# Kernel tuning notes

Hardware: AMD Instinct MI355X
Metric: run time of the kernel (lower is better)

## Reference

```python
import jax, jax.numpy as jnp
from jax import lax
import numpy as np

B = 16384
EPS = 1e-5


def conv2d(x, w, b, pad):
    # x: [N,C,H,W], w: [O,I,kh,kw]
    y = lax.conv_general_dilated(x, w, (1, 1), [(pad, pad), (pad, pad)],
                                 dimension_numbers=("NCHW", "OIHW", "NCHW"))
    return y + b[None, :, None, None]


def maxpool2(x):
    return lax.reduce_window(x, -jnp.inf, lax.max, (1, 1, 2, 2), (1, 1, 2, 2), "VALID")


def setup_inputs() -> dict:
    key = jax.random.key(0)
    ks = jax.random.split(key, 16)
    n = jax.random.normal
    return {
        "x": n(ks[0], (B, 1, 28, 28), dtype=jnp.float32),
        "conv1_w": n(ks[1], (8, 1, 3, 3), dtype=jnp.float32) * 0.2,
        "conv1_b": n(ks[2], (8,), dtype=jnp.float32) * 0.1,
        "conv2_w": n(ks[3], (16, 8, 3, 3), dtype=jnp.float32) * 0.1,
        "conv2_b": n(ks[4], (16,), dtype=jnp.float32) * 0.1,
        "s1_w": n(ks[5], (4, 2), dtype=jnp.float32) * 0.5,
        "s1_b": n(ks[6], (4,), dtype=jnp.float32) * 0.1,
        "s2_w": n(ks[7], (2, 4), dtype=jnp.float32) * 0.5,
        "s2_b": n(ks[8], (2,), dtype=jnp.float32) * 0.1,
        "filt_w": n(ks[9], (1, 1, 2, 2), dtype=jnp.float32) * 0.5,
        "filt_b": n(ks[10], (1,), dtype=jnp.float32) * 0.1,
        "fc1_w": n(ks[11], (64, 787), dtype=jnp.float32) * 0.03,
        "fc1_b": n(ks[12], (64,), dtype=jnp.float32) * 0.1,
        "fc2_w": n(ks[13], (4, 64), dtype=jnp.float32) * 0.1,
        "fc2_b": n(ks[14], (4,), dtype=jnp.float32) * 0.1,
        "bn_g": jnp.ones((4,), dtype=jnp.float32),
        "bn_b": jnp.zeros((4,), dtype=jnp.float32),
    }


def reference(x, conv1_w, conv1_b, conv2_w, conv2_b, s1_w, s1_b, s2_w, s2_b,
              filt_w, filt_b, fc1_w, fc1_b, fc2_w, fc2_b, bn_g, bn_b):
    bsz = x.shape[0]
    # feature extractor: conv3x3 -> relu -> maxpool2 (x2)
    f = maxpool2(jax.nn.relu(conv2d(x, conv1_w, conv1_b, 1)))        # [B,8,14,14]
    f = maxpool2(jax.nn.relu(conv2d(f, conv2_w, conv2_b, 1)))        # [B,16,7,7]
    flat = f.reshape(bsz, -1)                                        # [B,784]
    # sampler on first two features
    h = jnp.tanh(flat[:, :2] @ s1_w.T + s1_b)
    sampler_out = jax.nn.softmax(h @ s2_w.T + s2_b, axis=-1)         # [B,2]
    # conv filter: 2x2 stride-1 conv + sigmoid, mean over all patches
    logits = conv2d(x, filt_w, filt_b, 0)                            # [B,1,27,27]
    conv_out = jnp.mean(jax.nn.sigmoid(logits), axis=(1, 2, 3))[:, None]  # [B,1]
    combined = jnp.concatenate([flat, sampler_out, conv_out], axis=1)  # [B,787]
    out = jax.nn.relu(combined @ fc1_w.T + fc1_b) @ fc2_w.T + fc2_b    # [B,4]
    # BatchNorm1d, training mode (batch stats, biased variance)
    mu = jnp.mean(out, axis=0)
    var = jnp.var(out, axis=0)
    return (out - mu) * lax.rsqrt(var + EPS) * bn_g + bn_b
```

## Files before the change

kernel.cpp:

```cpp
#include <hip/hip_runtime.h>
#include <hip/hip_fp16.h>
#include <math.h>

#define NBATCH 16384
#define EPSV 1e-5f
#define IMGW 4

typedef short short8 __attribute__((ext_vector_type(8)));
typedef _Float16 half8_t __attribute__((ext_vector_type(8)));
typedef short short2v __attribute__((ext_vector_type(2)));
typedef float f32x4 __attribute__((ext_vector_type(4)));
union V8 { uint4 u; short8 s; };
union VH { uint4 u; half8_t h; };

__device__ __forceinline__ unsigned short f2bf(float f) {
    unsigned int x = __float_as_uint(f);
    return (unsigned short)((x + 0x7fffu + ((x >> 16) & 1u)) >> 16);
}
__device__ __forceinline__ __half2 u2h(unsigned int u) { return __builtin_bit_cast(__half2, u); }
__device__ __forceinline__ unsigned int h2u(__half2 h) { return __builtin_bit_cast(unsigned int, h); }

__global__ __launch_bounds__(256) void k_prep(
    const float* __restrict__ fc1w, const float* __restrict__ w2,
    const float* __restrict__ w1, const float* __restrict__ b1,
    unsigned short* __restrict__ wt, unsigned short* __restrict__ af16,
    unsigned int* __restrict__ w1h2, unsigned int* __restrict__ b1h2)
{
    int i = blockIdx.x * 256 + threadIdx.x;
    if (i < 51200) {
        int n = i / 800, k = i - n * 800;
        float v = (k < 787) ? fc1w[n * 787 + k] : 0.f;
        wt[i] = f2bf(v);
    } else if (i < 52736) {
        int a = i - 51200;
        int slot = a >> 7, rem = a & 127, oc = rem >> 3, ic = rem & 7;
        float v = (slot < 9) ? w2[oc * 72 + ic * 9 + slot] : 0.f;
        af16[a] = __half_as_ushort(__float2half(v));
    } else if (i < 52808) {
        int k = i - 52736;
        unsigned int hb = __half_as_ushort(__float2half(w1[k]));
        w1h2[k] = hb | (hb << 16);
    } else if (i < 52816) {
        int k = i - 52808;
        unsigned int hb = __half_as_ushort(__float2half(b1[k]));
        b1h2[k] = hb | (hb << 16);
    }
}

__global__ __launch_bounds__(256) void k_conv(
    const float* __restrict__ x,
    const float* __restrict__ s1w, const float* __restrict__ s1b,
    const float* __restrict__ s2w, const float* __restrict__ s2b,
    const float* __restrict__ fw, const float* __restrict__ fb,
    const float* __restrict__ b2,
    const unsigned short* __restrict__ Afg,
    const unsigned int* __restrict__ w1h2g,
    const unsigned int* __restrict__ b1h2g,
    unsigned short* __restrict__ comb)
{
    const int t = threadIdx.x;
    const int w = t >> 6, l = t & 63;

    __shared__ unsigned int sxu_all[4][30 * 18];
    __shared__ __align__(16) unsigned short sf1_all[4][16 * 136];
    __shared__ __align__(16) float scomb_all[4][800];
    __shared__ float ssm[27];
    __shared__ float sb2s[16];

    unsigned int* sxu = sxu_all[w];
    unsigned short* sf1 = sf1_all[w];
    float* scomb = scomb_all[w];

    if (t < 8) ssm[t] = s1w[t];
    else if (t < 12) ssm[t] = s1b[t - 8];
    else if (t < 20) ssm[t] = s2w[t - 12];
    else if (t < 22) ssm[t] = s2b[t - 20];
    else if (t < 26) ssm[t] = fw[t - 22];
    else if (t == 26) ssm[26] = fb[0];
    if (t >= 32 && t < 48) sb2s[t - 32] = b2[t - 32];
    __syncthreads();

    for (int i = l; i < 540; i += 64) sxu[i] = 0u;
    if (l < 60) {
        int R, C;
        if (l < 16)      { R = 0;      C = l; }
        else if (l < 32) { R = 15;     C = l - 16; }
        else if (l < 46) { R = l - 31; C = 0; }
        else             { R = l - 45; C = 15; }
        *reinterpret_cast<uint4*>(&sf1[R * 136 + C * 8]) = uint4{0u, 0u, 0u, 0u};
    }
    if (l < 16) scomb[784 + l] = 0.f;

    const __half2 fwh0 = __float2half2_rn(ssm[22]);
    const __half2 fwh1 = __float2half2_rn(ssm[23]);
    const __half2 fwh2 = __float2half2_rn(ssm[24]);
    const __half2 fwh3 = __float2half2_rn(ssm[25]);
    const __half2 fbh  = __float2half2_rn(ssm[26]);

    const int n = l & 15, g = l >> 4;
    const int qr = n & 7;
    const int q = (qr < 7) ? qr : 6;
    const int dr = n >> 3;
    int offs[3];
    VH af[3];
    #pragma unroll
    for (int s = 0; s < 3; ++s) {
        const int slot = s * 4 + g;
        const int u = slot / 3, v = slot - 3 * (slot / 3);
        offs[s] = (slot <= 8) ? (u * 136 + v * 8) : 0;
        af[s].u = *reinterpret_cast<const uint4*>(Afg + ((slot * 16 + n) << 3));
    }

    #pragma unroll 1
    for (int img = 0; img < IMGW; ++img) {
        const int b = (blockIdx.x * 4 + w) * IMGW + img;
        const float* xb = x + (size_t)b * 784;

        for (int u0 = l; u0 < 420; u0 += 64) {
            int r = u0 / 15, ww = u0 - (u0 / 15) * 15;
            __half2 h2;
            if (ww == 0)       h2 = __floats2half2_rn(0.f, xb[r * 28]);
            else if (ww == 14) h2 = __floats2half2_rn(xb[r * 28 + 27], 0.f);
            else               h2 = __floats2half2_rn(xb[r * 28 + 2 * ww - 1],
                                                      xb[r * 28 + 2 * ww]);
            sxu[(r + 1) * 18 + ww] = h2u(h2);
        }

        float fsum = 0.f;
        for (int u0 = l; u0 < 378; u0 += 64) {
            int r = u0 / 14, cp = u0 - (u0 / 14) * 14;
            unsigned int A1 = sxu[(r + 1) * 18 + cp], B1 = sxu[(r + 1) * 18 + cp + 1];
            unsigned int A2 = sxu[(r + 2) * 18 + cp], B2 = sxu[(r + 2) * 18 + cp + 1];
            __half2 al1 = u2h(__builtin_amdgcn_alignbit(B1, A1, 16));
            __half2 al2 = u2h(__builtin_amdgcn_alignbit(B2, A2, 16));
            __half2 acc = __hfma2(fwh0, al1,
                          __hfma2(fwh1, u2h(B1),
                          __hfma2(fwh2, al2,
                          __hfma2(fwh3, u2h(B2), fbh))));
            float2 f = __half22float2(acc);
            fsum += __frcp_rn(1.f + __expf(-f.x));
            if (cp < 13) fsum += __frcp_rn(1.f + __expf(-f.y));
        }
        #pragma unroll
        for (int off = 32; off > 0; off >>= 1)
            fsum += __shfl_xor(fsum, off, 64);

        for (int i = l; i < 196; i += 64) {
            const int p = i / 14, j = i - (i / 14) * 14;
            unsigned int A[4], B[4], M[4];
            #pragma unroll
            for (int u = 0; u < 4; ++u) {
                A[u] = sxu[(2 * p + u) * 18 + j];
                B[u] = sxu[(2 * p + u) * 18 + j + 1];
                M[u] = __builtin_amdgcn_alignbit(B[u], A[u], 16);
            }
            unsigned short outv[8];
            #pragma unroll
            for (int oc = 0; oc < 8; ++oc) {
                __half2 a0 = u2h(b1h2g[oc]), a1 = a0;
                #pragma unroll
                for (int u = 0; u < 3; ++u) {
                    #pragma unroll
                    for (int v = 0; v < 3; ++v) {
                        const __half2 wv = u2h(w1h2g[oc * 9 + u * 3 + v]);
                        const unsigned int p0 = (v == 0) ? A[u]     : ((v == 1) ? M[u]     : B[u]);
                        const unsigned int p1 = (v == 0) ? A[u + 1] : ((v == 1) ? M[u + 1] : B[u + 1]);
                        a0 = __hfma2(wv, u2h(p0), a0);
                        a1 = __hfma2(wv, u2h(p1), a1);
                    }
                }
                short2v s0 = __builtin_bit_cast(short2v, a0);
                short2v s1 = __builtin_bit_cast(short2v, a1);
                short2v mm = __builtin_elementwise_max(s0, s1);
                short m = mm[0] > mm[1] ? mm[0] : mm[1];
                if (m < 0) m = 0;
                outv[oc] = (unsigned short)m;
            }
            *reinterpret_cast<uint4*>(&sf1[(p + 1) * 136 + (j + 1) * 8]) =
                *reinterpret_cast<const uint4*>(outv);
        }

        for (int pp = 0; pp < 7; ++pp) {
            const int rbase = (2 * pp + dr) * 136 + (2 * q) * 8;
            f32x4 acc0 = {0.f, 0.f, 0.f, 0.f}, acc1 = {0.f, 0.f, 0.f, 0.f};
            #pragma unroll
            for (int s = 0; s < 3; ++s) {
                VH b0, b1v;
                b0.u  = *reinterpret_cast<const uint4*>(&sf1[rbase + offs[s]]);
                b1v.u = *reinterpret_cast<const uint4*>(&sf1[rbase + 8 + offs[s]]);
                acc0 = __builtin_amdgcn_mfma_f32_16x16x32_f16(af[s].h, b0.h, acc0, 0, 0, 0);
                acc1 = __builtin_amdgcn_mfma_f32_16x16x32_f16(af[s].h, b1v.h, acc1, 0, 0, 0);
            }
            #pragma unroll
            for (int i = 0; i < 4; ++i) {
                const float bias = sb2s[4 * g + i];
                float m = fmaxf(acc0[i], acc1[i]);
                m = fmaxf(m, __shfl_xor(m, 8, 64));
                if (n < 7)
                    scomb[(4 * g + i) * 49 + pp * 7 + q] = fmaxf(m + bias, 0.f);
            }
        }

        if (l == 0) {
            scomb[786] = fsum * (1.f / 729.f);
            float f0 = scomb[0], f1 = scomb[1];
            float h[4];
            #pragma unroll
            for (int k = 0; k < 4; ++k) {
                float y = fmaf(f0, ssm[k * 2], fmaf(f1, ssm[k * 2 + 1], ssm[8 + k]));
                float e = __expf(2.f * y);
                h[k] = (e - 1.f) * __frcp_rn(e + 1.f);
            }
            float l0 = ssm[20], l1 = ssm[21];
            #pragma unroll
            for (int k = 0; k < 4; ++k) {
                l0 = fmaf(h[k], ssm[12 + k], l0);
                l1 = fmaf(h[k], ssm[16 + k], l1);
            }
            float mx = fmaxf(l0, l1);
            float e0 = __expf(l0 - mx), e1 = __expf(l1 - mx);
            float inv = __frcp_rn(e0 + e1);
            scomb[784] = e0 * inv;
            scomb[785] = e1 * inv;
        }

        for (int u = l; u < 100; u += 64) {
            const float4* sp = reinterpret_cast<const float4*>(scomb);
            float4 f0 = sp[2 * u], f1 = sp[2 * u + 1];
            uint4 o;
            o.x = (unsigned int)f2bf(f0.x) | ((unsigned int)f2bf(f0.y) << 16);
            o.y = (unsigned int)f2bf(f0.z) | ((unsigned int)f2bf(f0.w) << 16);
            o.z = (unsigned int)f2bf(f1.x) | ((unsigned int)f2bf(f1.y) << 16);
            o.w = (unsigned int)f2bf(f1.z) | ((unsigned int)f2bf(f1.w) << 16);
            reinterpret_cast<uint4*>(comb)[(size_t)b * 100 + u] = o;
        }
    }
}

__global__ __launch_bounds__(256) void k_fc(
    const unsigned short* __restrict__ A,
    const unsigned short* __restrict__ Bw,
    const float* __restrict__ fc1b,
    const float* __restrict__ fc2w, const float* __restrict__ fc2b,
    float* __restrict__ out, float* __restrict__ part)
{
    __shared__ uint4 Asm[2][256];
    __shared__ uint4 Bsm[2][256];
    __shared__ float sh[64][68];
    __shared__ float sfc2[4][64];
    __shared__ float pacc[4][8];

    const int t = threadIdx.x;
    const int w = t >> 6, l = t & 63;
    const int blk = blockIdx.x;

    sfc2[t >> 6][t & 63] = fc2w[t];

    const int srow = t >> 2, skbp = t & 3;
    const int skbl = skbp ^ ((srow >> 1) & 3);
    const uint4* Ag = reinterpret_cast<const uint4*>(A) + ((size_t)blk * 64 + srow) * 100;
    const uint4* Bg = reinterpret_cast<const uint4*>(Bw) + (size_t)srow * 100;
    const int sidx = srow * 4 + skbp;

    const int arow = w * 16 + (l & 15);
    const int aidx = arow * 4 + ((l >> 4) ^ ((arow >> 1) & 3));
    int bidx[4];
    #pragma unroll
    for (int nf = 0; nf < 4; ++nf) {
        int nn = nf * 16 + (l & 15);
        bidx[nf] = nn * 4 + ((l >> 4) ^ ((nn >> 1) & 3));
    }

    f32x4 acc0 = {0.f, 0.f, 0.f, 0.f}, acc1 = acc0, acc2 = acc0, acc3 = acc0;

    Asm[0][sidx] = Ag[skbl];
    Bsm[0][sidx] = Bg[skbl];

    int buf = 0;
    for (int s = 0; s < 25; ++s) {
        __syncthreads();
        if (s < 24) {
            Asm[buf ^ 1][sidx] = Ag[(s + 1) * 4 + skbl];
            Bsm[buf ^ 1][sidx] = Bg[(s + 1) * 4 + skbl];
        }
        V8 av; av.u = Asm[buf][aidx];
        V8 b0; b0.u = Bsm[buf][bidx[0]];
        V8 b1; b1.u = Bsm[buf][bidx[1]];
        V8 b2; b2.u = Bsm[buf][bidx[2]];
        V8 b3; b3.u = Bsm[buf][bidx[3]];
        acc0 = __builtin_amdgcn_mfma_f32_16x16x32_bf16(av.s, b0.s, acc0, 0, 0, 0);
        acc1 = __builtin_amdgcn_mfma_f32_16x16x32_bf16(av.s, b1.s, acc1, 0, 0, 0);
        acc2 = __builtin_amdgcn_mfma_f32_16x16x32_bf16(av.s, b2.s, acc2, 0, 0, 0);
        acc3 = __builtin_amdgcn_mfma_f32_16x16x32_bf16(av.s, b3.s, acc3, 0, 0, 0);
        buf ^= 1;
    }

    {
        const int c0 = l & 15, r0 = w * 16 + (l >> 4) * 4;
        float fb0 = fc1b[c0], fb1 = fc1b[16 + c0], fb2 = fc1b[32 + c0], fb3 = fc1b[48 + c0];
        #pragma unroll
        for (int r = 0; r < 4; ++r) {
            sh[r0 + r][c0]      = fmaxf(acc0[r] + fb0, 0.f);
            sh[r0 + r][16 + c0] = fmaxf(acc1[r] + fb1, 0.f);
            sh[r0 + r][32 + c0] = fmaxf(acc2[r] + fb2, 0.f);
            sh[r0 + r][48 + c0] = fmaxf(acc3[r] + fb3, 0.f);
        }
    }
    __syncthreads();

    {
        const int row = t >> 2, oo = t & 3;
        float s = fc2b[oo];
        #pragma unroll 8
        for (int o = 0; o < 64; ++o)
            s = fmaf(sh[row][o], sfc2[oo][o], s);
        out[((size_t)blk * 64 + row) * 4 + oo] = s;

        float rs = s, rq = s * s;
        #pragma unroll
        for (int off = 4; off < 64; off <<= 1) {
            rs += __shfl_xor(rs, off, 64);
            rq += __shfl_xor(rq, off, 64);
        }
        if (l < 4) pacc[w][l] = rs;
        else if (l < 8) pacc[w][l] = rq;
    }
    __syncthreads();
    if (t < 8)
        part[blk * 8 + t] = pacc[0][t] + pacc[1][t] + pacc[2][t] + pacc[3][t];
}

__global__ void k_bnfinal(const float* __restrict__ part,
                          const float* __restrict__ g, const float* __restrict__ bb,
                          float* __restrict__ ss, int nblocks)
{
    const int t = threadIdx.x;
    float s[8];
    #pragma unroll
    for (int i = 0; i < 8; ++i) s[i] = 0.f;
    for (int idx = t; idx < nblocks; idx += 64)
        #pragma unroll
        for (int i = 0; i < 8; ++i) s[i] += part[idx * 8 + i];
    #pragma unroll
    for (int i = 0; i < 8; ++i)
        #pragma unroll
        for (int off = 32; off > 0; off >>= 1)
            s[i] += __shfl_xor(s[i], off, 64);
    if (t == 0) {
        const float invB = 1.f / 16384.f;
        #pragma unroll
        for (int j = 0; j < 4; ++j) {
            float mu = s[j] * invB;
            float var = s[4 + j] * invB - mu * mu;
            float sc = g[j] * rsqrtf(var + EPSV);
            ss[j] = sc;
            ss[4 + j] = bb[j] - mu * sc;
        }
    }
}

__global__ __launch_bounds__(256) void k_bnapply(const float* __restrict__ ss,
                                                 float* __restrict__ out)
{
    const int row = blockIdx.x * 256 + threadIdx.x;
    float4 v = reinterpret_cast<float4*>(out)[row];
    v.x = fmaf(v.x, ss[0], ss[4]);
    v.y = fmaf(v.y, ss[1], ss[5]);
    v.z = fmaf(v.z, ss[2], ss[6]);
    v.w = fmaf(v.w, ss[3], ss[7]);
    reinterpret_cast<float4*>(out)[row] = v;
}

__global__ __launch_bounds__(256) void k_transpose_fb(const float* __restrict__ in,
                                                      float* __restrict__ out)
{
    int i = blockIdx.x * 256 + threadIdx.x;
    if (i < 787 * 64) {
        int k = i >> 6, o = i & 63;
        out[i] = in[o * 787 + k];
    }
}

#define SF1F(ic, r, c) sf1[(ic) * 324 + (r) * 20 + (c)]

__global__ __launch_bounds__(256) void k_fused_fb(
    const float* __restrict__ x,
    const float* __restrict__ w1, const float* __restrict__ b1,
    const float* __restrict__ w2, const float* __restrict__ b2,
    const float* __restrict__ s1w, const float* __restrict__ s1b,
    const float* __restrict__ s2w, const float* __restrict__ s2b,
    const float* __restrict__ fw, const float* __restrict__ fb,
    const float* __restrict__ wt, const float* __restrict__ fc1b,
    const float* __restrict__ fc2w, const float* __restrict__ fc2b,
    float* __restrict__ pre)
{
    const int b = blockIdx.x;
    const int t = threadIdx.x;

    __shared__ float sxA[30][20];
    __shared__ float sxB[30][20];
    __shared__ float sf1[8 * 324];
    __shared__ float scomb[788];
    __shared__ float sw1[72];
    __shared__ float sb1[8];
    __shared__ float sw2p[16 * 76];
    __shared__ float sb2[16];
    __shared__ float sh1p[4][64];
    __shared__ float sh1[64];
    __shared__ float sred[4];
    __shared__ float ssm[27];

    for (int i = t; i < 600; i += 256) { (&sxA[0][0])[i] = 0.f; (&sxB[0][0])[i] = 0.f; }
    for (int i = t; i < 8 * 324; i += 256) sf1[i] = 0.f;
    if (t < 72) sw1[t] = w1[t];
    if (t < 8) sb1[t] = b1[t];
    for (int i = t; i < 1152; i += 256) {
        int oc = i / 72, rem = i - oc * 72;
        sw2p[oc * 76 + rem] = w2[i];
    }
    if (t < 16) sb2[t] = b2[t];
    if (t < 8) ssm[t] = s1w[t];
    else if (t < 12) ssm[t] = s1b[t - 8];
    else if (t < 20) ssm[t] = s2w[t - 12];
    else if (t < 22) ssm[t] = s2b[t - 20];
    else if (t < 26) ssm[t] = fw[t - 22];
    else if (t == 26) ssm[t] = fb[0];
    __syncthreads();

    const float* xb = x + (size_t)b * 784;
    for (int i = t; i < 784; i += 256) {
        int r = i / 28, c = i - (i / 28) * 28;
        float v = xb[i];
        int pr = r + 1, pc = c + 1;
        if (pc <= 15) sxA[pr][pc] = v;
        if (pc >= 14) sxB[pr][pc - 14] = v;
    }
    __syncthreads();

    {
        const float fw00 = ssm[22], fw01 = ssm[23], fw10 = ssm[24], fw11 = ssm[25];
        const float fbv = ssm[26];
        float fsum = 0.f;
        for (int i = t; i < 729; i += 256) {
            int r = i / 27, c = i - (i / 27) * 27;
            float x00, x01, x10, x11;
            if (c <= 13) {
                x00 = sxA[r + 1][c + 1]; x01 = sxA[r + 1][c + 2];
                x10 = sxA[r + 2][c + 1]; x11 = sxA[r + 2][c + 2];
            } else {
                int cb = c - 14;
                x00 = sxB[r + 1][cb + 1]; x01 = sxB[r + 1][cb + 2];
                x10 = sxB[r + 2][cb + 1]; x11 = sxB[r + 2][cb + 2];
            }
            float v = fbv;
            v = fmaf(x00, fw00, v); v = fmaf(x01, fw01, v);
            v = fmaf(x10, fw10, v); v = fmaf(x11, fw11, v);
            fsum += 1.f / (1.f + expf(-v));
        }
        #pragma unroll
        for (int off = 32; off > 0; off >>= 1)
            fsum += __shfl_xor(fsum, off, 64);
        if ((t & 63) == 0) sred[t >> 6] = fsum;
    }

    {
        const int half = t >> 7;
        const int id = t & 127;
        if (id < 112) {
            const int p = id >> 3, oc = id & 7;
            const float* base = half ? &sxB[0][0] : &sxA[0][0];
            float X[4][16];
            #pragma unroll
            for (int u = 0; u < 4; ++u) {
                const float4* rp = reinterpret_cast<const float4*>(base + (2 * p + u) * 20);
                float4 a = rp[0], bb4 = rp[1], c4 = rp[2], d4 = rp[3];
                X[u][0] = a.x;  X[u][1] = a.y;  X[u][2] = a.z;  X[u][3] = a.w;
                X[u][4] = bb4.x; X[u][5] = bb4.y; X[u][6] = bb4.z; X[u][7] = bb4.w;
                X[u][8] = c4.x;  X[u][9] = c4.y;  X[u][10] = c4.z; X[u][11] = c4.w;
                X[u][12] = d4.x; X[u][13] = d4.y; X[u][14] = d4.z; X[u][15] = d4.w;
            }
            float W[9];
            #pragma unroll
            for (int k = 0; k < 9; ++k) W[k] = sw1[oc * 9 + k];
            const float bias = sb1[oc];
            const int j0 = half * 7;
            #pragma unroll
            for (int jj = 0; jj < 7; ++jj) {
                float m = 0.f;
                #pragma unroll
                for (int dr = 0; dr < 2; ++dr)
                    #pragma unroll
                    for (int dc = 0; dc < 2; ++dc) {
                        float acc = bias;
                        #pragma unroll
                        for (int u = 0; u < 3; ++u)
                            #pragma unroll
                            for (int v = 0; v < 3; ++v)
                                acc = fmaf(X[dr + u][2 * jj + dc + v], W[u * 3 + v], acc);
                        m = fmaxf(m, acc);
                    }
                SF1F(oc, p + 1, j0 + jj + 1) = m;
            }
        }
    }
    __syncthreads();

    if (t < 112) {
        const int p = t >> 4, oc = t & 15;
        const float bias = sb2[oc];
        float acc[7][4];
        #pragma unroll
        for (int jj = 0; jj < 7; ++jj)
            #pragma unroll
            for (int s = 0; s < 4; ++s) acc[jj][s] = bias;
        for (int ic = 0; ic < 8; ++ic) {
            float X[4][16];
            #pragma unroll
            for (int u = 0; u < 4; ++u) {
                const float4* rp = reinterpret_cast<const float4*>(&SF1F(ic, 2 * p + u, 0));
                float4 a = rp[0], bb4 = rp[1], c4 = rp[2], d4 = rp[3];
                X[u][0] = a.x;  X[u][1] = a.y;  X[u][2] = a.z;  X[u][3] = a.w;
                X[u][4] = bb4.x; X[u][5] = bb4.y; X[u][6] = bb4.z; X[u][7] = bb4.w;
                X[u][8] = c4.x;  X[u][9] = c4.y;  X[u][10] = c4.z; X[u][11] = c4.w;
                X[u][12] = d4.x; X[u][13] = d4.y; X[u][14] = d4.z; X[u][15] = d4.w;
            }
            float W[9];
            #pragma unroll
            for (int k = 0; k < 9; ++k) W[k] = sw2p[oc * 76 + ic * 9 + k];
            #pragma unroll
            for (int jj = 0; jj < 7; ++jj)
                #pragma unroll
                for (int dr = 0; dr < 2; ++dr)
                    #pragma unroll
                    for (int dc = 0; dc < 2; ++dc)
                        #pragma unroll
                        for (int u = 0; u < 3; ++u)
                            #pragma unroll
                            for (int v = 0; v < 3; ++v)
                                acc[jj][dr * 2 + dc] =
                                    fmaf(X[dr + u][2 * jj + dc + v], W[u * 3 + v], acc[jj][dr * 2 + dc]);
        }
        #pragma unroll
        for (int jj = 0; jj < 7; ++jj) {
            float m = fmaxf(fmaxf(acc[jj][0], acc[jj][1]), fmaxf(acc[jj][2], acc[jj][3]));
            scomb[oc * 49 + p * 7 + jj] = fmaxf(m, 0.f);
        }
    }
    __syncthreads();

    if (t == 0) {
        scomb[786] = (sred[0] + sred[1] + sred[2] + sred[3]) * (1.f / 729.f);
        float f0 = scomb[0], f1 = scomb[1];
        float h[4];
        #pragma unroll
        for (int k = 0; k < 4; ++k)
            h[k] = tanhf(fmaf(f0, ssm[k * 2], fmaf(f1, ssm[k * 2 + 1], ssm[8 + k])));
        float l0 = ssm[20], l1 = ssm[21];
        #pragma unroll
        for (int k = 0; k < 4; ++k) {
            l0 = fmaf(h[k], ssm[12 + k], l0);
            l1 = fmaf(h[k], ssm[16 + k], l1);
        }
        float mx = fmaxf(l0, l1);
        float e0 = expf(l0 - mx), e1 = expf(l1 - mx);
        float inv = 1.f / (e0 + e1);
        scomb[784] = e0 * inv;
        scomb[785] = e1 * inv;
    }
    __syncthreads();

    {
        const int o = t & 63, w = t >> 6;
        const int k0 = w * 197;
        const int k1 = (w == 3) ? 787 : k0 + 197;
        const float* wp = wt + (size_t)k0 * 64 + o;
        float acc = 0.f;
        #pragma unroll 4
        for (int k = k0; k < k1; ++k) {
            acc = fmaf(scomb[k], *wp, acc);
            wp += 64;
        }
        sh1p[w][o] = acc;
    }
    __syncthreads();
    if (t < 64)
        sh1[t] = fmaxf(sh1p[0][t] + sh1p[1][t] + sh1p[2][t] + sh1p[3][t] + fc1b[t], 0.f);
    __syncthreads();

    {
        const int oo = t >> 6, lane = t & 63;
        float v = sh1[lane] * fc2w[oo * 64 + lane];
        #pragma unroll
        for (int off = 32; off > 0; off >>= 1)
            v += __shfl_xor(v, off, 64);
        if (lane == 0) pre[(size_t)b * 4 + oo] = v + fc2b[oo];
    }
}

__global__ __launch_bounds__(256) void k_bnstat_fb(const float* __restrict__ pre,
                                                   float* __restrict__ part)
{
    const int t = threadIdx.x;
    const int row = blockIdx.x * 256 + t;
    float4 v = reinterpret_cast<const float4*>(pre)[row];
    float s0 = v.x, s1 = v.y, s2 = v.z, s3 = v.w;
    float q0 = v.x * v.x, q1 = v.y * v.y, q2 = v.z * v.z, q3 = v.w * v.w;
    #pragma unroll
    for (int off = 32; off > 0; off >>= 1) {
        s0 += __shfl_xor(s0, off, 64);
        s1 += __shfl_xor(s1, off, 64);
        s2 += __shfl_xor(s2, off, 64);
        s3 += __shfl_xor(s3, off, 64);
        q0 += __shfl_xor(q0, off, 64);
        q1 += __shfl_xor(q1, off, 64);
        q2 += __shfl_xor(q2, off, 64);
        q3 += __shfl_xor(q3, off, 64);
    }
    __shared__ float acc[4][8];
    if ((t & 63) == 0) {
        int w = t >> 6;
        acc[w][0] = s0; acc[w][1] = s1; acc[w][2] = s2; acc[w][3] = s3;
        acc[w][4] = q0; acc[w][5] = q1; acc[w][6] = q2; acc[w][7] = q3;
    }
    __syncthreads();
    if (t < 8)
        part[blockIdx.x * 8 + t] = acc[0][t] + acc[1][t] + acc[2][t] + acc[3][t];
}

extern "C" void kernel_launch(void* const* d_in, const int* in_sizes, int n_in,
                              void* d_out, int out_size, void* d_ws, size_t ws_size,
                              hipStream_t stream)
{
    const float* x    = (const float*)d_in[0];
    const float* w1   = (const float*)d_in[1];
    const float* b1   = (const float*)d_in[2];
    const float* w2   = (const float*)d_in[3];
    const float* b2   = (const float*)d_in[4];
    const float* s1w  = (const float*)d_in[5];
    const float* s1b  = (const float*)d_in[6];
    const float* s2w  = (const float*)d_in[7];
    const float* s2b  = (const float*)d_in[8];
    const float* fw   = (const float*)d_in[9];
    const float* fb   = (const float*)d_in[10];
    const float* fc1w = (const float*)d_in[11];
    const float* fc1b = (const float*)d_in[12];
    const float* fc2w = (const float*)d_in[13];
    const float* fc2b = (const float*)d_in[14];
    const float* bng  = (const float*)d_in[15];
    const float* bnb  = (const float*)d_in[16];

    float* out = (float*)d_out;

    const size_t COMB_BYTES = (size_t)NBATCH * 800 * 2;
    const size_t WT_BYTES   = 64 * 800 * 2;
    const size_t AF16_BYTES = 1536 * 2;
    const size_t W1H2_BYTES = 72 * 4;
    const size_t B1H2_BYTES = 8 * 4;
    const size_t PART_BYTES = 256 * 8 * 4;
    const size_t NEED = COMB_BYTES + WT_BYTES + AF16_BYTES + W1H2_BYTES +
                        B1H2_BYTES + PART_BYTES + 32;

    if (ws_size >= NEED) {
        char* p = (char*)d_ws;
        unsigned short* comb = (unsigned short*)p;                     p += COMB_BYTES;
        unsigned short* wtbf = (unsigned short*)p;                     p += WT_BYTES;
        unsigned short* af16 = (unsigned short*)p;                     p += AF16_BYTES;
        unsigned int*   w1h2 = (unsigned int*)p;                       p += W1H2_BYTES;
        unsigned int*   b1h2 = (unsigned int*)p;                       p += B1H2_BYTES;
        float*          part = (float*)p;                              p += PART_BYTES;
        float*          ss   = (float*)p;

        k_prep<<<207, 256, 0, stream>>>(fc1w, w2, w1, b1, wtbf, af16, w1h2, b1h2);
        k_conv<<<NBATCH / (4 * IMGW), 256, 0, stream>>>(x, s1w, s1b, s2w, s2b, fw, fb, b2,
                                                        af16, w1h2, b1h2, comb);
        k_fc<<<256, 256, 0, stream>>>(comb, wtbf, fc1b, fc2w, fc2b, out, part);
        k_bnfinal<<<1, 64, 0, stream>>>(part, bng, bnb, ss, 256);
        k_bnapply<<<64, 256, 0, stream>>>(ss, out);
    } else {
        float* part = (float*)d_ws;
        float* ss   = part + 512;
        float* wt   = ss + 8;

        k_transpose_fb<<<197, 256, 0, stream>>>(fc1w, wt);
        k_fused_fb<<<NBATCH, 256, 0, stream>>>(x, w1, b1, w2, b2, s1w, s1b, s2w, s2b,
                                               fw, fb, wt, fc1b, fc2w, fc2b, out);
        k_bnstat_fb<<<64, 256, 0, stream>>>(out, part);
        k_bnfinal<<<1, 64, 0, stream>>>(part, bng, bnb, ss, 64);
        k_bnapply<<<64, 256, 0, stream>>>(ss, out);
    }
}
```

Measured before the change: 105.3 us.

## Shrink conv kernel LDS, batch input loads, halve images per wave

The conv kernel now holds its per-wave combined feature buffer as bf16 instead of fp32, which cuts shared memory use. It pads the input tile stride to 17 words to change the LDS bank pattern. All input pixel loads are issued before any LDS store so global latency overlaps, and the launch bounds request 5 blocks per CU. IMGW drops from 4 to 2, which doubles the grid, trading more blocks and repeated per-block setup for better occupancy and latency hiding.

```diff
diff --git a/kernel.cpp b/kernel.cpp
--- a/kernel.cpp
+++ b/kernel.cpp
@@ -4,7 +4,7 @@
 
 #define NBATCH 16384
 #define EPSV 1e-5f
-#define IMGW 4
+#define IMGW 2
 
 typedef short short8 __attribute__((ext_vector_type(8)));
 typedef _Float16 half8_t __attribute__((ext_vector_type(8)));
@@ -16,6 +16,9 @@
 __device__ __forceinline__ unsigned short f2bf(float f) {
     unsigned int x = __float_as_uint(f);
     return (unsigned short)((x + 0x7fffu + ((x >> 16) & 1u)) >> 16);
+}
+__device__ __forceinline__ float bf2f(unsigned short u) {
+    return __uint_as_float(((unsigned int)u) << 16);
 }
 __device__ __forceinline__ __half2 u2h(unsigned int u) { return __builtin_bit_cast(__half2, u); }
 __device__ __forceinline__ unsigned int h2u(__half2 h) { return __builtin_bit_cast(unsigned int, h); }
@@ -47,7 +50,9 @@
     }
 }
 
-__global__ __launch_bounds__(256) void k_conv(
+#define SXS 17
+
+__global__ __launch_bounds__(256, 5) void k_conv(
     const float* __restrict__ x,
     const float* __restrict__ s1w, const float* __restrict__ s1b,
     const float* __restrict__ s2w, const float* __restrict__ s2b,
@@ -61,15 +66,15 @@
     const int t = threadIdx.x;
     const int w = t >> 6, l = t & 63;
 
-    __shared__ unsigned int sxu_all[4][30 * 18];
+    __shared__ unsigned int sxu_all[4][30 * SXS];
     __shared__ __align__(16) unsigned short sf1_all[4][16 * 136];
-    __shared__ __align__(16) float scomb_all[4][800];
+    __shared__ __align__(16) unsigned short scombh_all[4][800];
     __shared__ float ssm[27];
     __shared__ float sb2s[16];
 
     unsigned int* sxu = sxu_all[w];
     unsigned short* sf1 = sf1_all[w];
-    float* scomb = scomb_all[w];
+    unsigned short* scombh = scombh_all[w];
 
     if (t < 8) ssm[t] = s1w[t];
     else if (t < 12) ssm[t] = s1b[t - 8];
@@ -80,7 +85,7 @@
     if (t >= 32 && t < 48) sb2s[t - 32] = b2[t - 32];
     __syncthreads();
 
-    for (int i = l; i < 540; i += 64) sxu[i] = 0u;
+    for (int i = l; i < 30 * SXS; i += 64) sxu[i] = 0u;
     if (l < 60) {
         int R, C;
         if (l < 16)      { R = 0;      C = l; }
@@ -89,7 +94,7 @@
         else             { R = l - 45; C = 15; }
         *reinterpret_cast<uint4*>(&sf1[R * 136 + C * 8]) = uint4{0u, 0u, 0u, 0u};
     }
-    if (l < 16) scomb[784 + l] = 0.f;
+    if (l < 16) scombh[784 + l] = 0;
 
     const __half2 fwh0 = __float2half2_rn(ssm[22]);
     const __half2 fwh1 = __float2half2_rn(ssm[23]);
@@ -111,26 +116,41 @@
         af[s].u = *reinterpret_cast<const uint4*>(Afg + ((slot * 16 + n) << 3));
     }
 
+    int srow[7], sww[7];
+    #pragma unroll
+    for (int k = 0; k < 7; ++k) {
+        int u0 = l + k * 64;
+        srow[k] = u0 / 15;
+        sww[k]  = u0 - srow[k] * 15;
+    }
+
     #pragma unroll 1
     for (int img = 0; img < IMGW; ++img) {
         const int b = (blockIdx.x * 4 + w) * IMGW + img;
         const float* xb = x + (size_t)b * 784;
 
-        for (int u0 = l; u0 < 420; u0 += 64) {
-            int r = u0 / 15, ww = u0 - (u0 / 15) * 15;
-            __half2 h2;
-            if (ww == 0)       h2 = __floats2half2_rn(0.f, xb[r * 28]);
-            else if (ww == 14) h2 = __floats2half2_rn(xb[r * 28 + 27], 0.f);
-            else               h2 = __floats2half2_rn(xb[r * 28 + 2 * ww - 1],
-                                                      xb[r * 28 + 2 * ww]);
-            sxu[(r + 1) * 18 + ww] = h2u(h2);
+        float xlo[7], xhi[7];
+        #pragma unroll
+        for (int k = 0; k < 7; ++k) {
+            const int u0 = l + k * 64;
+            if (u0 < 420) {
+                const float* base = xb + srow[k] * 28;
+                xlo[k] = (sww[k] == 0)  ? 0.f : base[2 * sww[k] - 1];
+                xhi[k] = (sww[k] == 14) ? 0.f : base[2 * sww[k]];
+            }
+        }
+        #pragma unroll
+        for (int k = 0; k < 7; ++k) {
+            const int u0 = l + k * 64;
+            if (u0 < 420)
+                sxu[(srow[k] + 1) * SXS + sww[k]] = h2u(__floats2half2_rn(xlo[k], xhi[k]));
         }
 
         float fsum = 0.f;
         for (int u0 = l; u0 < 378; u0 += 64) {
             int r = u0 / 14, cp = u0 - (u0 / 14) * 14;
-            unsigned int A1 = sxu[(r + 1) * 18 + cp], B1 = sxu[(r + 1) * 18 + cp + 1];
-            unsigned int A2 = sxu[(r + 2) * 18 + cp], B2 = sxu[(r + 2) * 18 + cp + 1];
+            unsigned int A1 = sxu[(r + 1) * SXS + cp], B1 = sxu[(r + 1) * SXS + cp + 1];
+            unsigned int A2 = sxu[(r + 2) * SXS + cp], B2 = sxu[(r + 2) * SXS + cp + 1];
             __half2 al1 = u2h(__builtin_amdgcn_alignbit(B1, A1, 16));
             __half2 al2 = u2h(__builtin_amdgcn_alignbit(B2, A2, 16));
             __half2 acc = __hfma2(fwh0, al1,
@@ -150,8 +170,8 @@
             unsigned int A[4], B[4], M[4];
             #pragma unroll
             for (int u = 0; u < 4; ++u) {
-                A[u] = sxu[(2 * p + u) * 18 + j];
-                B[u] = sxu[(2 * p + u) * 18 + j + 1];
+                A[u] = sxu[(2 * p + u) * SXS + j];
+                B[u] = sxu[(2 * p + u) * SXS + j + 1];
                 M[u] = __builtin_amdgcn_alignbit(B[u], A[u], 16);
             }
             unsigned short outv[8];
@@ -197,13 +217,13 @@
                 float m = fmaxf(acc0[i], acc1[i]);
                 m = fmaxf(m, __shfl_xor(m, 8, 64));
                 if (n < 7)
-                    scomb[(4 * g + i) * 49 + pp * 7 + q] = fmaxf(m + bias, 0.f);
+                    scombh[(4 * g + i) * 49 + pp * 7 + q] = f2bf(fmaxf(m + bias, 0.f));
             }
         }
 
         if (l == 0) {
-            scomb[786] = fsum * (1.f / 729.f);
-            float f0 = scomb[0], f1 = scomb[1];
+            scombh[786] = f2bf(fsum * (1.f / 729.f));
+            float f0 = bf2f(scombh[0]), f1 = bf2f(scombh[1]);
             float h[4];
             #pragma unroll
             for (int k = 0; k < 4; ++k) {
@@ -220,18 +240,12 @@
             float mx = fmaxf(l0, l1);
             float e0 = __expf(l0 - mx), e1 = __expf(l1 - mx);
             float inv = __frcp_rn(e0 + e1);
-            scomb[784] = e0 * inv;
-            scomb[785] = e1 * inv;
+            scombh[784] = f2bf(e0 * inv);
+            scombh[785] = f2bf(e1 * inv);
         }
 
         for (int u = l; u < 100; u += 64) {
-            const float4* sp = reinterpret_cast<const float4*>(scomb);
-            float4 f0 = sp[2 * u], f1 = sp[2 * u + 1];
-            uint4 o;
-            o.x = (unsigned int)f2bf(f0.x) | ((unsigned int)f2bf(f0.y) << 16);
-            o.y = (unsigned int)f2bf(f0.z) | ((unsigned int)f2bf(f0.w) << 16);
-            o.z = (unsigned int)f2bf(f1.x) | ((unsigned int)f2bf(f1.y) << 16);
-            o.w = (unsigned int)f2bf(f1.z) | ((unsigned int)f2bf(f1.w) << 16);
+            uint4 o = *reinterpret_cast<const uint4*>(&scombh[u * 8]);
             reinterpret_cast<uint4*>(comb)[(size_t)b * 100 + u] = o;
         }
     }
```

New measurement: 109.4 us. 3.9% more time.
